# Optimization experiments

Measured on AMD Instinct MI355X. Metric: run time of the kernel, lower is better.

## Reference

```python
import jax, jax.numpy as jnp
import numpy as np

K_COMP = 32   # num_components
HID = 64      # hidden_dim
OBS = 32      # obs_dim
T_LEN = 500   # sequence length


def setup_inputs() -> dict:
    key = jax.random.key(0)
    ks = jax.random.split(key, 6)
    data = jax.random.normal(ks[0], (T_LEN, OBS), dtype=jnp.float32)
    transition_logits = 0.1 * jax.random.normal(ks[1], (K_COMP, K_COMP), dtype=jnp.float32)
    transition_matrix = jnp.eye(HID, dtype=jnp.float32) + 0.05 * jax.random.normal(ks[2], (K_COMP, HID, HID), dtype=jnp.float32)
    log_transition_noise = 0.1 * jax.random.normal(ks[3], (HID,), dtype=jnp.float32)
    observation_matrix = 0.3 * jax.random.normal(ks[4], (HID, OBS), dtype=jnp.float32)
    log_obs_noise = 0.1 * jax.random.normal(ks[5], (OBS,), dtype=jnp.float32)
    return {"data": data, "transition_logits": transition_logits,
            "transition_matrix": transition_matrix, "log_transition_noise": log_transition_noise,
            "observation_matrix": observation_matrix, "log_obs_noise": log_obs_noise}


def _obs_update(log_w, mu, P, C, R, y):
    # Observation model: y = x @ C + eps, eps ~ N(0, R). Per-component Kalman update.
    D = C.shape[1]
    PC = jnp.einsum('khg,gd->khd', P, C)              # (K,H,D)
    S = jnp.einsum('hd,khe->kde', C, PC) + R          # (K,D,D) innovation cov
    S = 0.5 * (S + S.swapaxes(-1, -2))
    v = y[None, :] - mu @ C                           # (K,D) innovation
    a = jnp.linalg.solve(S, v[..., None])[..., 0]     # S^{-1} v
    Kg = jnp.linalg.solve(S, PC.swapaxes(-1, -2)).swapaxes(-1, -2)  # (K,H,D)
    logdet = jnp.linalg.slogdet(S)[1]
    ll = -0.5 * (D * jnp.log(2.0 * jnp.pi) + logdet + jnp.sum(v * a, axis=-1))
    mu_new = mu + jnp.einsum('khd,kd->kh', Kg, v)
    P_new = P - jnp.einsum('khd,kde,kge->khg', Kg, S, Kg)
    P_new = 0.5 * (P_new + P_new.swapaxes(-1, -2))
    return log_w + ll, mu_new, P_new


def _predict_mm(log_w, mu, P, A, Q, trans_log):
    # Propagate each (prev comp k -> new comp j) then moment-match over k per j.
    m = jnp.einsum('jhg,kg->jkh', A, mu)                      # (J,K,H)
    Pp = jnp.einsum('jhg,kgf,jef->jkhe', A, P, A) + Q         # (J,K,H,H)
    lw = trans_log.T + log_w[None, :]                          # (J,K): log_w[k] + logT[k,j]
    new_lw = jax.scipy.special.logsumexp(lw, axis=1)           # (J,)
    r = jax.nn.softmax(lw, axis=1)                             # (J,K) mixture weights
    mu_new = jnp.einsum('jk,jkh->jh', r, m)
    dm = m - mu_new[:, None, :]
    P_new = jnp.einsum('jk,jkhe->jhe', r, Pp) + jnp.einsum('jk,jkh,jke->jhe', r, dm, dm)
    P_new = 0.5 * (P_new + P_new.swapaxes(-1, -2))
    return new_lw, mu_new, P_new


def reference(data, transition_logits, transition_matrix, log_transition_noise,
              observation_matrix, log_obs_noise):
    K = transition_matrix.shape[0]
    H = transition_matrix.shape[1]
    trans_log = jax.nn.log_softmax(transition_logits, axis=-1)   # (K,K)
    Q = jnp.diag(jnp.exp(log_transition_noise))                  # (H,H)
    R = jnp.diag(jnp.exp(log_obs_noise))                         # (D,D)
    C = observation_matrix                                       # (H,D)

    # t = 0: s_{-1} fixed to 0 -> prior over s_0 is row 0; x_0 ~ N(0, I)
    log_w = trans_log[0]
    mu = jnp.zeros((K, H), dtype=data.dtype)
    P = jnp.broadcast_to(jnp.eye(H, dtype=data.dtype), (K, H, H))
    log_w, mu, P = _obs_update(log_w, mu, P, C, R, data[0])

    def step(carry, y):
        lw, mu_c, P_c = carry
        lw, mu_c, P_c = _predict_mm(lw, mu_c, P_c, transition_matrix, Q, trans_log)
        lw, mu_c, P_c = _obs_update(lw, mu_c, P_c, C, R, y)
        return (lw, mu_c, P_c), None

    (log_w, mu, P), _ = jax.lax.scan(step, (log_w, mu, P), data[1:])
    return jax.scipy.special.logsumexp(log_w)
```

## Files before the change

### kernel.cpp

```cpp
#include <hip/hip_runtime.h>
#include <math.h>

#define KC 32
#define HD 64
#define OB 32
#define TLEN 500
#define NB 32
#define NT 256
#define LOG2PI 1.8378770664093453f

#define WS_LW0 64
#define WS_LW1 96
#define WS_MU0 128
#define WS_MU1 2176
#define WS_PPB 4224

__device__ __forceinline__ unsigned bfp(float x){
  unsigned u = __float_as_uint(x);
  return (u + 0x7FFFu + ((u >> 16) & 1u)) >> 16;
}
__device__ __forceinline__ unsigned packbf(float a, float b){
  return bfp(a) | (bfp(b) << 16);
}
__device__ __forceinline__ float lo16(unsigned u){ return __uint_as_float(u << 16); }
__device__ __forceinline__ float hi16(unsigned u){ return __uint_as_float(u & 0xFFFF0000u); }

__device__ __forceinline__ void gridbar(unsigned* cnt, unsigned* gen) {
  __syncthreads();
  if (threadIdx.x == 0) {
    __threadfence();
    unsigned g = __hip_atomic_load(gen, __ATOMIC_RELAXED, __HIP_MEMORY_SCOPE_AGENT);
    unsigned a = __hip_atomic_fetch_add(cnt, 1u, __ATOMIC_RELAXED, __HIP_MEMORY_SCOPE_AGENT);
    if (a == NB - 1) {
      __hip_atomic_store(cnt, 0u, __ATOMIC_RELAXED, __HIP_MEMORY_SCOPE_AGENT);
      __hip_atomic_fetch_add(gen, 1u, __ATOMIC_RELEASE, __HIP_MEMORY_SCOPE_AGENT);
    } else {
      while (__hip_atomic_load(gen, __ATOMIC_RELAXED, __HIP_MEMORY_SCOPE_AGENT) == g)
        __builtin_amdgcn_s_sleep(1);
    }
    __threadfence();
  }
  __syncthreads();
}

__global__ __launch_bounds__(NT, 1) void slds_kernel(
    const float* __restrict__ gdata, const float* __restrict__ gtl,
    const float* __restrict__ gA, const float* __restrict__ gltn,
    const float* __restrict__ gC, const float* __restrict__ glon,
    float* __restrict__ gout, float* __restrict__ ws)
{
  __shared__ __align__(16) float At[4096];
  __shared__ __align__(16) float Ct[2048];
  __shared__ __align__(16) float Cn[64*33];
  __shared__ __align__(16) float Pm[64*68];
  __shared__ __align__(16) float Sc[64*68];
  __shared__ __align__(16) float WL[64*5 + 4];
  __shared__ __align__(16) float mbp[256];
  __shared__ __align__(16) float mubar[64];
  __shared__ __align__(16) float muL[64];
  __shared__ float tl[32], qd[64], rdv[32], yv[32];
  __shared__ float Gbuf[16], cmPb[16];

  const int j = blockIdx.x, tid = threadIdx.x;
  unsigned* cnt = (unsigned*)ws;
  unsigned* gen = ((unsigned*)ws) + 1;
  unsigned short* ppb = (unsigned short*)(ws + WS_PPB);

  for (int e = tid; e < 4096; e += NT) { int r = e >> 6, g = e & 63; At[g*64 + r] = gA[j*4096 + e]; }
  for (int e = tid; e < 2048; e += NT) { int hh = e >> 5, dd = e & 31; Ct[dd*64 + hh] = gC[e]; Cn[hh*33 + dd] = gC[e]; }
  if (tid < 64) qd[tid] = expf(gltn[tid]);
  if (tid < 32) rdv[tid] = expf(glon[tid]);
  if (tid < 32) {
    float mx = -1e30f;
    for (int i = 0; i < 32; ++i) mx = fmaxf(mx, gtl[tid*32 + i]);
    float s = 0.f;
    for (int i = 0; i < 32; ++i) s += expf(gtl[tid*32 + i] - mx);
    tl[tid] = gtl[tid*32 + j] - (mx + logf(s));
  }
  __syncthreads();

  const int h  = tid >> 2, gq = tid & 3;
  const int r0 = (tid >> 4) << 2, c0 = (tid & 15) << 2;
  const int km = tid >> 3, seg = tid & 7;

  #pragma unroll 1
  for (int t = 0; t < TLEN; ++t) {
    float4 Preg[4];
    float mu_h = 0.f, base_lw;
    float llacc = 0.f;

    if (t == 0) {
      if (tid < 32) yv[tid] = gdata[tid];
      if (tid < 64) muL[tid] = 0.f;
      #pragma unroll
      for (int u = 0; u < 4; ++u) {
        int gb = gq*16 + 4*u;
        float4 vv = make_float4(0.f,0.f,0.f,0.f);
        if (h == gb  ) vv.x = 1.f;
        if (h == gb+1) vv.y = 1.f;
        if (h == gb+2) vv.z = 1.f;
        if (h == gb+3) vv.w = 1.f;
        Preg[u] = vv;
      }
      base_lw = tl[0];
      __syncthreads();
    } else {
      const float* lwR = (t & 1) ? (ws + WS_LW0) : (ws + WS_LW1);
      const float* muR = (t & 1) ? (ws + WS_MU0) : (ws + WS_MU1);
      const uint4* pp4 = (const uint4*)(ppb + ((t & 1) ? 0u : 131072u));

      if (tid < 32) yv[tid] = gdata[t*32 + tid];

      const float4* mup = (const float4*)(muR + km*64 + seg*8);
      float4 m0 = mup[0], m1 = mup[1];

      float av[32];
      #pragma unroll
      for (int k = 0; k < 32; ++k) av[k] = tl[k] + lwR[k];
      float mx = av[0];
      #pragma unroll
      for (int k = 1; k < 32; ++k) mx = fmaxf(mx, av[k]);

      const int u4i = tid*2;
      uint4 b0a[8], b1a[8];
      #pragma unroll
      for (int p = 0; p < 8; ++p) { b0a[p] = pp4[p*512 + u4i]; b1a[p] = pp4[p*512 + u4i + 1]; }

      float ssum = 0.f;
      #pragma unroll
      for (int k = 0; k < 32; ++k) { av[k] = expf(av[k] - mx); ssum += av[k]; }
      float inv = 1.f / ssum;
      base_lw = mx + logf(ssum);

      float4 acc[4];
      #pragma unroll
      for (int u = 0; u < 4; ++u) acc[u] = make_float4(0.f,0.f,0.f,0.f);
      #pragma unroll
      for (int k = 0; k < 32; ++k) {
        uint4 b0 = b0a[k & 7], b1 = b1a[k & 7];
        if (k < 24) { b0a[k & 7] = pp4[(k+8)*512 + u4i]; b1a[k & 7] = pp4[(k+8)*512 + u4i + 1]; }
        float rk = av[k] * inv;
        acc[0].x += rk*lo16(b0.x); acc[0].y += rk*hi16(b0.x);
        acc[0].z += rk*lo16(b0.y); acc[0].w += rk*hi16(b0.y);
        acc[1].x += rk*lo16(b0.z); acc[1].y += rk*hi16(b0.z);
        acc[1].z += rk*lo16(b0.w); acc[1].w += rk*hi16(b0.w);
        acc[2].x += rk*lo16(b1.x); acc[2].y += rk*hi16(b1.x);
        acc[2].z += rk*lo16(b1.y); acc[2].w += rk*hi16(b1.y);
        acc[3].x += rk*lo16(b1.z); acc[3].y += rk*hi16(b1.z);
        acc[3].z += rk*lo16(b1.w); acc[3].w += rk*hi16(b1.w);
      }

      {
        float rk2 = av[km] * inv;
        m0.x *= rk2; m0.y *= rk2; m0.z *= rk2; m0.w *= rk2;
        m1.x *= rk2; m1.y *= rk2; m1.z *= rk2; m1.w *= rk2;
        #pragma unroll
        for (int mk = 8; mk < 64; mk <<= 1) {
          m0.x += __shfl_xor(m0.x, mk); m0.y += __shfl_xor(m0.y, mk);
          m0.z += __shfl_xor(m0.z, mk); m0.w += __shfl_xor(m0.w, mk);
          m1.x += __shfl_xor(m1.x, mk); m1.y += __shfl_xor(m1.y, mk);
          m1.z += __shfl_xor(m1.z, mk); m1.w += __shfl_xor(m1.w, mk);
        }
        if ((tid & 56) == 0) {
          int w = tid >> 6;
          *(float4*)&mbp[w*64 + seg*8]     = m0;
          *(float4*)&mbp[w*64 + seg*8 + 4] = m1;
        }
      }
      __syncthreads();
      if (tid < 64) mubar[tid] = mbp[tid] + mbp[64+tid] + mbp[128+tid] + mbp[192+tid];
      __syncthreads();

      {
        float mh_ = mubar[h];
        #pragma unroll
        for (int u = 0; u < 4; ++u) {
          float4 mc = *(const float4*)&mubar[gq*16 + u*4];
          acc[u].x -= mh_*mc.x; acc[u].y -= mh_*mc.y;
          acc[u].z -= mh_*mc.z; acc[u].w -= mh_*mc.w;
          *(float4*)&Pm[h*68 + gq*16 + u*4] = acc[u];
        }
        float mp = 0.f;
        #pragma unroll
        for (int i = 0; i < 16; ++i) { int g = gq*16 + i; mp += At[g*64 + h] * mubar[g]; }
        mp += __shfl_xor(mp, 1); mp += __shfl_xor(mp, 2);
        mu_h = mp;
      }
      __syncthreads();

      {
        float gacc[4][4] = {};
        for (int g = 0; g < 64; ++g) {
          float4 a = *(const float4*)&At[g*64 + r0];
          float4 b = *(const float4*)&Pm[g*68 + c0];
          float avv[4] = {a.x,a.y,a.z,a.w};
          float bvv[4] = {b.x,b.y,b.z,b.w};
          #pragma unroll
          for (int ii = 0; ii < 4; ++ii)
            #pragma unroll
            for (int jj = 0; jj < 4; ++jj) gacc[ii][jj] += avv[ii]*bvv[jj];
        }
        #pragma unroll
        for (int jj = 0; jj < 4; ++jj) {
          float4 col = make_float4(gacc[0][jj], gacc[1][jj], gacc[2][jj], gacc[3][jj]);
          *(float4*)&Sc[(c0+jj)*68 + r0] = col;
        }
      }
      __syncthreads();

      {
        float gacc[4][4] = {};
        for (int g = 0; g < 64; ++g) {
          float4 a = *(const float4*)&At[g*64 + r0];
          float4 b = *(const float4*)&Sc[g*68 + c0];
          float avv[4] = {a.x,a.y,a.z,a.w};
          float bvv[4] = {b.x,b.y,b.z,b.w};
          #pragma unroll
          for (int ii = 0; ii < 4; ++ii)
            #pragma unroll
            for (int jj = 0; jj < 4; ++jj) gacc[ii][jj] += avv[ii]*bvv[jj];
        }
        if (r0 == c0) {
          gacc[0][0] += qd[r0]; gacc[1][1] += qd[r0+1];
          gacc[2][2] += qd[r0+2]; gacc[3][3] += qd[r0+3];
        }
        #pragma unroll
        for (int ii = 0; ii < 4; ++ii)
          *(float4*)&Pm[(r0+ii)*68 + c0] = make_float4(gacc[ii][0], gacc[ii][1], gacc[ii][2], gacc[ii][3]);
      }
      if (gq == 0) muL[h] = mu_h;
      __syncthreads();

      #pragma unroll
      for (int u = 0; u < 4; ++u) Preg[u] = *(const float4*)&Pm[h*68 + gq*16 + 4*u];
    }

    #pragma unroll 1
    for (int rnd = 0; rnd < 8; ++rnd) {
      const int d0 = rnd * 4;
      float wv[4];
      #pragma unroll
      for (int i = 0; i < 4; ++i) {
        const float4* cc = (const float4*)&Ct[(d0+i)*64 + gq*16];
        float wi = 0.f;
        #pragma unroll
        for (int u = 0; u < 4; ++u) {
          float4 c4 = cc[u]; float4 p = Preg[u];
          wi += p.x*c4.x + p.y*c4.y + p.z*c4.z + p.w*c4.w;
        }
        wv[i] = wi;
      }
      #pragma unroll
      for (int i = 0; i < 4; ++i) { wv[i] += __shfl_xor(wv[i], 1); wv[i] += __shfl_xor(wv[i], 2); }
      if (gq == 0) {
        WL[h*5+0]=wv[0]; WL[h*5+1]=wv[1]; WL[h*5+2]=wv[2]; WL[h*5+3]=wv[3];
      }
      {
        float cmp_ = Cn[h*33 + d0 + gq] * muL[h];
        cmp_ += __shfl_xor(cmp_, 4); cmp_ += __shfl_xor(cmp_, 8);
        cmp_ += __shfl_xor(cmp_, 16); cmp_ += __shfl_xor(cmp_, 32);
        if ((tid & 60) == 0) cmPb[(tid >> 6)*4 + gq] = cmp_;
      }
      __syncthreads();

      if (tid < 64) {
        int q = tid >> 4, ii = (tid >> 2) & 3, jj = tid & 3;
        float g_ = 0.f;
        #pragma unroll
        for (int hh = 0; hh < 16; ++hh) {
          int hq = q*16 + hh;
          g_ += Cn[hq*33 + d0 + ii] * WL[hq*5 + jj];
        }
        g_ += __shfl_xor(g_, 16); g_ += __shfl_xor(g_, 32);
        if (tid < 16) Gbuf[tid] = g_;
      }
      __syncthreads();

      {
        float G10=Gbuf[4],  G20=Gbuf[8],  G21=Gbuf[9];
        float G30=Gbuf[12], G31=Gbuf[13], G32=Gbuf[14];
        float s00=Gbuf[0]+rdv[d0],  s11=Gbuf[5]+rdv[d0+1];
        float s22=Gbuf[10]+rdv[d0+2], s33=Gbuf[15]+rdv[d0+3];
        float cm0=cmPb[0]+cmPb[4]+cmPb[8]+cmPb[12];
        float cm1=cmPb[1]+cmPb[5]+cmPb[9]+cmPb[13];
        float cm2=cmPb[2]+cmPb[6]+cmPb[10]+cmPb[14];
        float cm3=cmPb[3]+cmPb[7]+cmPb[11]+cmPb[15];
        float v0_=yv[d0]-cm0, v1_=yv[d0+1]-cm1, v2_=yv[d0+2]-cm2, v3_=yv[d0+3]-cm3;

        float L00=sqrtf(s00), rr0=1.f/L00;
        float L10=G10*rr0, L20=G20*rr0, L30=G30*rr0;
        float L11=sqrtf(s11-L10*L10), rr1=1.f/L11;
        float L21=(G21-L20*L10)*rr1, L31=(G31-L30*L10)*rr1;
        float L22=sqrtf(s22-L20*L20-L21*L21), rr2=1.f/L22;
        float L32=(G32-L30*L20-L31*L21)*rr2;
        float L33=sqrtf(s33-L30*L30-L31*L31-L32*L32), rr3=1.f/L33;
        llacc += 2.f*logf(L00*L11*L22*L33);

        float m00=rr0, m11=rr1, m22=rr2, m33=rr3;
        float m10=-rr1*(L10*m00);
        float m20=-rr2*(L20*m00+L21*m10);
        float m21=-rr2*(L21*m11);
        float m30=-rr3*(L30*m00+L31*m10+L32*m20);
        float m31=-rr3*(L31*m11+L32*m21);
        float m32=-rr3*(L32*m22);

        float si00=m00*m00+m10*m10+m20*m20+m30*m30;
        float si01=m10*m11+m20*m21+m30*m31;
        float si02=m20*m22+m30*m32;
        float si03=m30*m33;
        float si11=m11*m11+m21*m21+m31*m31;
        float si12=m21*m22+m31*m32;
        float si13=m31*m33;
        float si22=m22*m22+m32*m32;
        float si23=m32*m33;
        float si33=m33*m33;

        float uu0=si00*v0_+si01*v1_+si02*v2_+si03*v3_;
        float uu1=si01*v0_+si11*v1_+si12*v2_+si13*v3_;
        float uu2=si02*v0_+si12*v1_+si22*v2_+si23*v3_;
        float uu3=si03*v0_+si13*v1_+si23*v2_+si33*v3_;
        llacc += v0_*uu0 + v1_*uu1 + v2_*uu2 + v3_*uu3;

        float wr0=wv[0], wr1=wv[1], wr2=wv[2], wr3=wv[3];
        float zr0=wr0*si00+wr1*si01+wr2*si02+wr3*si03;
        float zr1=wr0*si01+wr1*si11+wr2*si12+wr3*si13;
        float zr2=wr0*si02+wr1*si12+wr2*si22+wr3*si23;
        float zr3=wr0*si03+wr1*si13+wr2*si23+wr3*si33;

        #pragma unroll
        for (int u = 0; u < 4; ++u) {
          int gb = gq*16 + u*4;
          Preg[u].x -= zr0*WL[(gb+0)*5+0]+zr1*WL[(gb+0)*5+1]+zr2*WL[(gb+0)*5+2]+zr3*WL[(gb+0)*5+3];
          Preg[u].y -= zr0*WL[(gb+1)*5+0]+zr1*WL[(gb+1)*5+1]+zr2*WL[(gb+1)*5+2]+zr3*WL[(gb+1)*5+3];
          Preg[u].z -= zr0*WL[(gb+2)*5+0]+zr1*WL[(gb+2)*5+1]+zr2*WL[(gb+2)*5+2]+zr3*WL[(gb+2)*5+3];
          Preg[u].w -= zr0*WL[(gb+3)*5+0]+zr1*WL[(gb+3)*5+1]+zr2*WL[(gb+3)*5+2]+zr3*WL[(gb+3)*5+3];
        }
        mu_h += wr0*uu0 + wr1*uu1 + wr2*uu2 + wr3*uu3;
        if (gq == 0) muL[h] = mu_h;
      }
      __syncthreads();
    }
    float lw_j = base_lw - 0.5f * (OB * LOG2PI + llacc);

    #pragma unroll
    for (int u = 0; u < 4; ++u) *(float4*)&Pm[h*68 + gq*16 + 4*u] = Preg[u];
    __syncthreads();
    {
      float* lwW = (t & 1) ? (ws + WS_LW1) : (ws + WS_LW0);
      float* muW = (t & 1) ? (ws + WS_MU1) : (ws + WS_MU0);
      uint4* ppW = (uint4*)(ppb + ((t & 1) ? 131072u : 0u)) + (size_t)j*512;
      float mh = muL[h];
      unsigned pk[8];
      #pragma unroll
      for (int u = 0; u < 4; ++u) {
        int gb = gq*16 + 4*u;
        float4 pv = Preg[u];
        float4 pt = make_float4(Pm[(gb+0)*68 + h], Pm[(gb+1)*68 + h],
                                Pm[(gb+2)*68 + h], Pm[(gb+3)*68 + h]);
        float4 m4 = *(const float4*)&muL[gb];
        float ox = 0.5f*(pv.x + pt.x) + mh*m4.x;
        float oy = 0.5f*(pv.y + pt.y) + mh*m4.y;
        float oz = 0.5f*(pv.z + pt.z) + mh*m4.z;
        float ow = 0.5f*(pv.w + pt.w) + mh*m4.w;
        pk[u*2]   = packbf(ox, oy);
        pk[u*2+1] = packbf(oz, ow);
      }
      ppW[h*8 + gq*2]     = make_uint4(pk[0], pk[1], pk[2], pk[3]);
      ppW[h*8 + gq*2 + 1] = make_uint4(pk[4], pk[5], pk[6], pk[7]);
      if (gq == 0) muW[j*64 + h] = mu_h;
      if (tid == 0) lwW[j] = lw_j;
    }
    gridbar(cnt, gen);
  }

  if (j == 0 && tid == 0) {
    const float* lw = ((TLEN - 1) & 1) ? (ws + WS_LW1) : (ws + WS_LW0);
    float mx = -1e30f;
    for (int k = 0; k < KC; ++k) mx = fmaxf(mx, lw[k]);
    float s = 0.f;
    for (int k = 0; k < KC; ++k) s += expf(lw[k] - mx);
    gout[0] = mx + logf(s);
  }
}

extern "C" void kernel_launch(void* const* d_in, const int* in_sizes, int n_in,
                              void* d_out, int out_size, void* d_ws, size_t ws_size,
                              hipStream_t stream) {
  const float* gdata = (const float*)d_in[0];
  const float* gtl   = (const float*)d_in[1];
  const float* gA    = (const float*)d_in[2];
  const float* gltn  = (const float*)d_in[3];
  const float* gC    = (const float*)d_in[4];
  const float* glon  = (const float*)d_in[5];
  float* ws = (float*)d_ws;

  hipMemsetAsync(d_ws, 0, 256, stream);
  hipLaunchKernelGGL(slds_kernel, dim3(NB), dim3(NT), 0, stream,
                     gdata, gtl, gA, gltn, gC, glon, (float*)d_out, ws);
}
```

Before: 16.29 ms.

## Replace grid barrier with per-block step flags and relaxed atomic exchange

Removes the counter/generation grid barrier and its thread fences. Each block now waits for a vmcnt drain, then publishes a per-block step counter; consumers poll the 32 producer flags before reading the double-buffered weights, means and covariances. Shared-buffer reads and writes become relaxed agent-scope 64-bit and 32-bit atomics so that no fences are needed. The intent is to shorten the per-timestep synchronisation latency across 500 sequential steps. The cost is narrower 64-bit loads instead of 128-bit loads and polling on 32 flags. Correctness depends on the vmcnt drain plus relaxed atomic ordering.

```diff
diff --git a/kernel.cpp b/kernel.cpp
--- a/kernel.cpp
+++ b/kernel.cpp
@@ -15,6 +15,8 @@
 #define WS_MU1 2176
 #define WS_PPB 4224
 
+typedef unsigned long long ull;
+
 __device__ __forceinline__ unsigned bfp(float x){
   unsigned u = __float_as_uint(x);
   return (u + 0x7FFFu + ((u >> 16) & 1u)) >> 16;
@@ -25,22 +27,17 @@
 __device__ __forceinline__ float lo16(unsigned u){ return __uint_as_float(u << 16); }
 __device__ __forceinline__ float hi16(unsigned u){ return __uint_as_float(u & 0xFFFF0000u); }
 
-__device__ __forceinline__ void gridbar(unsigned* cnt, unsigned* gen) {
-  __syncthreads();
-  if (threadIdx.x == 0) {
-    __threadfence();
-    unsigned g = __hip_atomic_load(gen, __ATOMIC_RELAXED, __HIP_MEMORY_SCOPE_AGENT);
-    unsigned a = __hip_atomic_fetch_add(cnt, 1u, __ATOMIC_RELAXED, __HIP_MEMORY_SCOPE_AGENT);
-    if (a == NB - 1) {
-      __hip_atomic_store(cnt, 0u, __ATOMIC_RELAXED, __HIP_MEMORY_SCOPE_AGENT);
-      __hip_atomic_fetch_add(gen, 1u, __ATOMIC_RELEASE, __HIP_MEMORY_SCOPE_AGENT);
-    } else {
-      while (__hip_atomic_load(gen, __ATOMIC_RELAXED, __HIP_MEMORY_SCOPE_AGENT) == g)
-        __builtin_amdgcn_s_sleep(1);
-    }
-    __threadfence();
-  }
-  __syncthreads();
+__device__ __forceinline__ ull ald64(const ull* p){
+  return __hip_atomic_load(p, __ATOMIC_RELAXED, __HIP_MEMORY_SCOPE_AGENT);
+}
+__device__ __forceinline__ void ast64(ull* p, ull v){
+  __hip_atomic_store(p, v, __ATOMIC_RELAXED, __HIP_MEMORY_SCOPE_AGENT);
+}
+__device__ __forceinline__ unsigned ald32(const unsigned* p){
+  return __hip_atomic_load(p, __ATOMIC_RELAXED, __HIP_MEMORY_SCOPE_AGENT);
+}
+__device__ __forceinline__ void ast32(unsigned* p, unsigned v){
+  __hip_atomic_store(p, v, __ATOMIC_RELAXED, __HIP_MEMORY_SCOPE_AGENT);
 }
 
 __global__ __launch_bounds__(NT, 1) void slds_kernel(
@@ -58,12 +55,11 @@
   __shared__ __align__(16) float mbp[256];
   __shared__ __align__(16) float mubar[64];
   __shared__ __align__(16) float muL[64];
-  __shared__ float tl[32], qd[64], rdv[32], yv[32];
+  __shared__ float tl[32], lwb[32], qd[64], rdv[32], yv[32];
   __shared__ float Gbuf[16], cmPb[16];
 
   const int j = blockIdx.x, tid = threadIdx.x;
-  unsigned* cnt = (unsigned*)ws;
-  unsigned* gen = ((unsigned*)ws) + 1;
+  unsigned* flags = (unsigned*)ws;
   unsigned short* ppb = (unsigned short*)(ws + WS_PPB);
 
   for (int e = tid; e < 4096; e += NT) { int r = e >> 6, g = e & 63; At[g*64 + r] = gA[j*4096 + e]; }
@@ -105,26 +101,34 @@
       base_lw = tl[0];
       __syncthreads();
     } else {
-      const float* lwR = (t & 1) ? (ws + WS_LW0) : (ws + WS_LW1);
-      const float* muR = (t & 1) ? (ws + WS_MU0) : (ws + WS_MU1);
-      const uint4* pp4 = (const uint4*)(ppb + ((t & 1) ? 0u : 131072u));
-
-      if (tid < 32) yv[tid] = gdata[t*32 + tid];
-
-      const float4* mup = (const float4*)(muR + km*64 + seg*8);
-      float4 m0 = mup[0], m1 = mup[1];
+      const unsigned* lwR = (const unsigned*)(ws + ((t & 1) ? WS_LW0 : WS_LW1));
+      const ull* muR = (const ull*)(ws + ((t & 1) ? WS_MU0 : WS_MU1));
+      const ull* pp8 = (const ull*)(ppb + ((t & 1) ? 0u : 131072u));
+
+      if (tid < 32) {
+        while (ald32(&flags[tid]) < (unsigned)t) __builtin_amdgcn_s_sleep(1);
+        lwb[tid] = tl[tid] + __uint_as_float(ald32(lwR + tid));
+        yv[tid] = gdata[t*32 + tid];
+      }
+      __syncthreads();
+
+      const ull* mup = muR + ((size_t)km*64 + seg*8) / 2;
+      ull mq0 = ald64(mup), mq1 = ald64(mup+1), mq2 = ald64(mup+2), mq3 = ald64(mup+3);
 
       float av[32];
       #pragma unroll
-      for (int k = 0; k < 32; ++k) av[k] = tl[k] + lwR[k];
+      for (int k = 0; k < 32; ++k) av[k] = lwb[k];
       float mx = av[0];
       #pragma unroll
       for (int k = 1; k < 32; ++k) mx = fmaxf(mx, av[k]);
 
-      const int u4i = tid*2;
-      uint4 b0a[8], b1a[8];
-      #pragma unroll
-      for (int p = 0; p < 8; ++p) { b0a[p] = pp4[p*512 + u4i]; b1a[p] = pp4[p*512 + u4i + 1]; }
+      const int qb = tid * 4;
+      ull qa[8][4];
+      #pragma unroll
+      for (int p = 0; p < 8; ++p) {
+        #pragma unroll
+        for (int q = 0; q < 4; ++q) qa[p][q] = ald64(pp8 + p*1024 + qb + q);
+      }
 
       float ssum = 0.f;
       #pragma unroll
@@ -137,21 +141,32 @@
       for (int u = 0; u < 4; ++u) acc[u] = make_float4(0.f,0.f,0.f,0.f);
       #pragma unroll
       for (int k = 0; k < 32; ++k) {
-        uint4 b0 = b0a[k & 7], b1 = b1a[k & 7];
-        if (k < 24) { b0a[k & 7] = pp4[(k+8)*512 + u4i]; b1a[k & 7] = pp4[(k+8)*512 + u4i + 1]; }
+        ull q0 = qa[k&7][0], q1 = qa[k&7][1], q2 = qa[k&7][2], q3 = qa[k&7][3];
+        if (k < 24) {
+          #pragma unroll
+          for (int q = 0; q < 4; ++q) qa[k&7][q] = ald64(pp8 + (k+8)*1024 + qb + q);
+        }
         float rk = av[k] * inv;
-        acc[0].x += rk*lo16(b0.x); acc[0].y += rk*hi16(b0.x);
-        acc[0].z += rk*lo16(b0.y); acc[0].w += rk*hi16(b0.y);
-        acc[1].x += rk*lo16(b0.z); acc[1].y += rk*hi16(b0.z);
-        acc[1].z += rk*lo16(b0.w); acc[1].w += rk*hi16(b0.w);
-        acc[2].x += rk*lo16(b1.x); acc[2].y += rk*hi16(b1.x);
-        acc[2].z += rk*lo16(b1.y); acc[2].w += rk*hi16(b1.y);
-        acc[3].x += rk*lo16(b1.z); acc[3].y += rk*hi16(b1.z);
-        acc[3].z += rk*lo16(b1.w); acc[3].w += rk*hi16(b1.w);
+        unsigned a0 = (unsigned)q0, a1 = (unsigned)(q0 >> 32);
+        unsigned b0 = (unsigned)q1, b1 = (unsigned)(q1 >> 32);
+        unsigned c0_ = (unsigned)q2, c1 = (unsigned)(q2 >> 32);
+        unsigned d0_ = (unsigned)q3, d1 = (unsigned)(q3 >> 32);
+        acc[0].x += rk*lo16(a0); acc[0].y += rk*hi16(a0);
+        acc[0].z += rk*lo16(a1); acc[0].w += rk*hi16(a1);
+        acc[1].x += rk*lo16(b0); acc[1].y += rk*hi16(b0);
+        acc[1].z += rk*lo16(b1); acc[1].w += rk*hi16(b1);
+        acc[2].x += rk*lo16(c0_); acc[2].y += rk*hi16(c0_);
+        acc[2].z += rk*lo16(c1); acc[2].w += rk*hi16(c1);
+        acc[3].x += rk*lo16(d0_); acc[3].y += rk*hi16(d0_);
+        acc[3].z += rk*lo16(d1); acc[3].w += rk*hi16(d1);
       }
 
       {
         float rk2 = av[km] * inv;
+        float4 m0 = make_float4(__uint_as_float((unsigned)mq0), __uint_as_float((unsigned)(mq0>>32)),
+                                __uint_as_float((unsigned)mq1), __uint_as_float((unsigned)(mq1>>32)));
+        float4 m1 = make_float4(__uint_as_float((unsigned)mq2), __uint_as_float((unsigned)(mq2>>32)),
+                                __uint_as_float((unsigned)mq3), __uint_as_float((unsigned)(mq3>>32)));
         m0.x *= rk2; m0.y *= rk2; m0.z *= rk2; m0.w *= rk2;
         m1.x *= rk2; m1.y *= rk2; m1.z *= rk2; m1.w *= rk2;
         #pragma unroll
@@ -346,9 +361,9 @@
     for (int u = 0; u < 4; ++u) *(float4*)&Pm[h*68 + gq*16 + 4*u] = Preg[u];
     __syncthreads();
     {
-      float* lwW = (t & 1) ? (ws + WS_LW1) : (ws + WS_LW0);
-      float* muW = (t & 1) ? (ws + WS_MU1) : (ws + WS_MU0);
-      uint4* ppW = (uint4*)(ppb + ((t & 1) ? 131072u : 0u)) + (size_t)j*512;
+      unsigned* lwW = (unsigned*)(ws + ((t & 1) ? WS_LW1 : WS_LW0));
+      unsigned* muW = (unsigned*)(ws + ((t & 1) ? WS_MU1 : WS_MU0));
+      ull* ppW = (ull*)(ppb + ((t & 1) ? 131072u : 0u)) + (size_t)j*1024 + tid*4;
       float mh = muL[h];
       unsigned pk[8];
       #pragma unroll
@@ -365,21 +380,32 @@
         pk[u*2]   = packbf(ox, oy);
         pk[u*2+1] = packbf(oz, ow);
       }
-      ppW[h*8 + gq*2]     = make_uint4(pk[0], pk[1], pk[2], pk[3]);
-      ppW[h*8 + gq*2 + 1] = make_uint4(pk[4], pk[5], pk[6], pk[7]);
-      if (gq == 0) muW[j*64 + h] = mu_h;
-      if (tid == 0) lwW[j] = lw_j;
+      ast64(ppW+0, (ull)pk[0] | ((ull)pk[1] << 32));
+      ast64(ppW+1, (ull)pk[2] | ((ull)pk[3] << 32));
+      ast64(ppW+2, (ull)pk[4] | ((ull)pk[5] << 32));
+      ast64(ppW+3, (ull)pk[6] | ((ull)pk[7] << 32));
+      if (gq == 0) ast32(&muW[j*64 + h], __float_as_uint(mu_h));
+      if (tid == 0) ast32(&lwW[j], __float_as_uint(lw_j));
     }
-    gridbar(cnt, gen);
+    asm volatile("s_waitcnt vmcnt(0)" ::: "memory");
+    __syncthreads();
+    if (tid == 0) ast32(&flags[j], (unsigned)(t + 1));
   }
 
-  if (j == 0 && tid == 0) {
-    const float* lw = ((TLEN - 1) & 1) ? (ws + WS_LW1) : (ws + WS_LW0);
-    float mx = -1e30f;
-    for (int k = 0; k < KC; ++k) mx = fmaxf(mx, lw[k]);
-    float s = 0.f;
-    for (int k = 0; k < KC; ++k) s += expf(lw[k] - mx);
-    gout[0] = mx + logf(s);
+  if (j == 0) {
+    if (tid < 32) {
+      while (ald32(&flags[tid]) < (unsigned)TLEN) __builtin_amdgcn_s_sleep(1);
+    }
+    __syncthreads();
+    if (tid == 0) {
+      const unsigned* lw = (const unsigned*)(ws + (((TLEN - 1) & 1) ? WS_LW1 : WS_LW0));
+      float mx = -1e30f;
+      float v[KC];
+      for (int k = 0; k < KC; ++k) { v[k] = __uint_as_float(ald32(lw + k)); mx = fmaxf(mx, v[k]); }
+      float s = 0.f;
+      for (int k = 0; k < KC; ++k) s += expf(v[k] - mx);
+      gout[0] = mx + logf(s);
+    }
   }
 }
 
```

After: 16.81 ms. 3.2% more time.
